# Performance work log

Hardware: AMD Instinct MI355X
Metric: run time of the kernel (lower is better)

## Reference

```python
import jax, jax.numpy as jnp
import numpy as np

B, L, R, H, TE = 4, 256, 64, 768, 100
TH = 0.5  # all four thresholds default to 0.5


def extract_first_embeddings(tok, start_probs, end_probs, threshold):
    """For each token i with start_prob>th, pair it with the nearest end index j>=i
    with end_prob>th; span embedding = mean(tok[i:j+1]). Valid spans are packed
    (in order) into a [b, l, h] table padded with zeros, with a [b, l] validity mask.
    Vectorized, jit-friendly reconstruction of the repo's span extractor."""
    b, l, h = tok.shape
    ar = jnp.arange(l)
    starts = start_probs > threshold            # [b, l]
    ends = end_probs > threshold                # [b, l]
    end_pos = jnp.where(ends, ar[None, :], l)   # l = sentinel 'no end'
    next_end = jax.lax.cummin(end_pos, axis=1, reverse=True)  # first end >= i
    valid = starts & (next_end < l)             # [b, l]
    j = jnp.minimum(next_end, l - 1)
    # inclusive span mean via prefix sums: mean = (csum[j+1] - csum[i]) / (j-i+1)
    csum0 = jnp.concatenate([jnp.zeros((b, 1, h), tok.dtype), jnp.cumsum(tok, axis=1)], axis=1)
    upper = jnp.take_along_axis(csum0, (j + 1)[:, :, None], axis=1)  # [b, l, h]
    lower = csum0[:, :-1]                                             # csum0[:, i]
    span_len = (j - ar[None, :] + 1).astype(tok.dtype)[:, :, None]
    span_emb = (upper - lower) / span_len
    # pack valid spans to the front (pad_sequence-style), pad with zeros to length l
    rank = jnp.cumsum(valid, axis=1) - 1
    rank_safe = jnp.where(valid, rank, l)       # dump invalids into extra slot l
    padded = jnp.zeros((b, l + 1, h), tok.dtype).at[
        jnp.arange(b)[:, None], rank_safe
    ].set(jnp.where(valid[:, :, None], span_emb, 0.0))[:, :l]
    num = valid.sum(axis=1)
    mask = ar[None, :] < num[:, None]
    return padded, mask


def setup_inputs() -> dict:
    key = jax.random.key(0)
    ks = jax.random.split(key, 12)
    s = 0.02
    return {
        "embs": jax.random.normal(ks[0], (B, L, H), jnp.float32),
        "h_gs": jax.random.normal(ks[1], (B, H), jnp.float32),
        "rel_embs": jax.random.normal(ks[2], (R, H), jnp.float32),
        "rel_transe_embs": jax.random.normal(ks[3], (R, TE), jnp.float32),
        "fc_w": jax.random.normal(ks[4], (8, H), jnp.float32) * s,
        "fc_b": jax.random.normal(ks[5], (8,), jnp.float32) * s,
        "Wm": jax.random.normal(ks[6], (10, H, H), jnp.float32) * s,
        "Wb": jax.random.normal(ks[7], (10, H), jnp.float32) * s,
        "V_w": jax.random.normal(ks[8], (H,), jnp.float32) * s,
        "V_b": jax.random.normal(ks[9], (1,), jnp.float32) * s,
        "rproj_w": jax.random.normal(ks[10], (TE, H), jnp.float32) * s,
        "rproj_b": jax.random.normal(ks[11], (H,), jnp.float32) * s,
    }


def _forward(embs, h_gs, rel_embs, rel_transe_embs, fc_w, fc_b, Wm, Wb, V_w, V_b, rproj_w, rproj_b):
    sig = jax.nn.sigmoid
    b_rel = rel_transe_embs @ rproj_w + rproj_b            # [r, h] r_proj

    # ---- first-stage scalar heads on tokens ----
    f_sub_s = embs @ fc_w[0] + fc_b[0]                     # [b, l]
    f_sub_e = embs @ fc_w[1] + fc_b[1]
    b_obj_s = embs @ fc_w[2] + fc_b[2]
    b_obj_e = embs @ fc_w[3] + fc_b[3]

    f_pad, f_mask = extract_first_embeddings(embs, sig(f_sub_s), sig(f_sub_e), TH)
    b_pad, b_mask = extract_first_embeddings(embs, sig(b_obj_s), sig(b_obj_e), TH)
    f_s_w = (f_pad @ Wm[0] + Wb[0]) * f_mask[:, :, None].astype(embs.dtype)  # f_W_s
    b_o_w = (b_pad @ Wm[1] + Wb[1]) * b_mask[:, :, None].astype(embs.dtype)  # b_W_s

    # ---- relation attention: tanh(W_r rel + W_g hg + W_x tok), broadcast [b,l,r,h] ----
    def rel_attn(rel, iWr, iWg, iWx):
        relp = rel @ Wm[iWr] + Wb[iWr]                     # [r, h]
        hgp = h_gs @ Wm[iWg] + Wb[iWg]                     # [b, h]
        tokp = embs @ Wm[iWx] + Wb[iWx]                    # [b, l, h]
        e = jnp.tanh(tokp[:, :, None, :] + relp[None, None, :, :] + hgp[:, None, None, :])
        v = e @ V_w + V_b                                  # [b, l, r]
        A = jax.nn.softmax(v, axis=1)                      # softmax over tokens
        C = jnp.einsum('blr,blh->brh', A, embs)            # relation context
        return C

    f_C = rel_attn(rel_embs, 2, 3, 4)
    b_C = rel_attn(b_rel, 5, 6, 7)

    # ---- pairwise table heads; Hijk = Hik[:,:,None]+C[:,None]+tok[:,:,None] is linear
    # under the scalar head, so compute logits without materializing [b,l,r,h] ----
    f_Hik = f_s_w + embs @ Wm[8] + Wb[8]                   # [b, l, h] (f_Wx2)
    b_Hik = b_o_w + embs @ Wm[9] + Wb[9]                   # (b_Wx2)

    def pair_logits(Hik, C, i):
        t = (Hik + embs) @ fc_w[i]                         # [b, l]
        return t[:, :, None] + (C @ fc_w[i])[:, None, :] + fc_b[i]  # [b, l, r]

    f_obj_s = pair_logits(f_Hik, f_C, 4)
    f_obj_e = pair_logits(f_Hik, f_C, 5)
    b_sub_s = pair_logits(b_Hik, b_C, 6)
    b_sub_e = pair_logits(b_Hik, b_C, 7)

    # order: forward(sub_s, sub_e, obj_s, obj_e), backward(obj_s, obj_e, sub_s, sub_e)
    return (f_sub_s, f_sub_e, f_obj_s, f_obj_e, b_obj_s, b_obj_e, b_sub_s, b_sub_e)


def reference(embs, h_gs, rel_embs, rel_transe_embs, fc_w, fc_b, Wm, Wb, V_w, V_b, rproj_w, rproj_b):
    return _forward(embs, h_gs, rel_embs, rel_transe_embs, fc_w, fc_b, Wm, Wb, V_w, V_b, rproj_w, rproj_b)
```

## Files before the change

### kernel.cpp

```cpp
#include <hip/hip_runtime.h>
#include <cstddef>

using u16 = unsigned short;
typedef __attribute__((ext_vector_type(8))) short bf16x8;
typedef __attribute__((ext_vector_type(4))) short bf16x4;
typedef __attribute__((ext_vector_type(4))) float f32x4;

constexpr int kB = 4, kL = 256, kR = 64, kH = 768, kTE = 100;
constexpr size_t HH = (size_t)kH * kH;

constexpr size_t OFF_FSS = 0;
constexpr size_t OFF_FSE = OFF_FSS + kB * kL;
constexpr size_t OFF_FOS = OFF_FSE + kB * kL;
constexpr size_t OFF_FOE = OFF_FOS + (size_t)kB * kL * kR;
constexpr size_t OFF_BOS = OFF_FOE + (size_t)kB * kL * kR;
constexpr size_t OFF_BOE = OFF_BOS + kB * kL;
constexpr size_t OFF_BSS = OFF_BOE + kB * kL;
constexpr size_t OFF_BSE = OFF_BSS + (size_t)kB * kL * kR;

constexpr size_t WS_WTALL   = 0;
constexpr size_t WS_EMBSB   = WS_WTALL   + 10 * HH / 2;
constexpr size_t WS_RELEMBB = WS_EMBSB   + (1024 * 768) / 2;
constexpr size_t WS_HGSB    = WS_RELEMBB + (64 * 768) / 2;
constexpr size_t WS_FPADB   = WS_HGSB    + (4 * 768) / 2;
constexpr size_t WS_BPADB   = WS_FPADB   + (1024 * 768) / 2;
constexpr size_t WS_BRELB   = WS_BPADB   + (1024 * 768) / 2;
constexpr size_t WS_TOKPB   = WS_BRELB   + (64 * 768) / 2;
constexpr size_t WS_RELPF   = WS_TOKPB   + (2 * 1024 * 768) / 2;
constexpr size_t WS_RELPB   = WS_RELPF   + 64 * 768;
constexpr size_t WS_HGPF    = WS_RELPB   + 64 * 768;
constexpr size_t WS_HGPB    = WS_HGPF    + 4 * 768;
constexpr size_t WS_DD      = WS_HGPB    + 4 * 768;
constexpr size_t WS_UA      = WS_DD      + 4 * 1024;
constexpr size_t WS_UB      = WS_UA      + 4 * 768;
constexpr size_t WS_CC      = WS_UB      + 4 * 768;
constexpr size_t WS_FMASK   = WS_CC      + 8;
constexpr size_t WS_BMASK   = WS_FMASK   + 1024;
constexpr size_t WS_C4      = WS_BMASK   + 1024;
constexpr size_t WS_C5      = WS_C4 + 256;
constexpr size_t WS_C6      = WS_C5 + 256;
constexpr size_t WS_C7      = WS_C6 + 256;

__device__ inline float fast_rcp(float x) {
#if __has_builtin(__builtin_amdgcn_rcpf)
    return __builtin_amdgcn_rcpf(x);
#else
    return 1.f / x;
#endif
}
__device__ inline float fast_exp2(float x) {
#if __has_builtin(__builtin_amdgcn_exp2f)
    return __builtin_amdgcn_exp2f(x);
#else
    return __exp2f(x);
#endif
}
__device__ inline u16 f2bf(float x) {
    union { float f; unsigned u; } v; v.f = x;
    unsigned r = v.u + 0x7FFFu + ((v.u >> 16) & 1u);
    return (u16)(r >> 16);
}
__device__ inline float bf2f(u16 x) {
    union { unsigned u; float f; } v; v.u = ((unsigned)x) << 16;
    return v.f;
}

__global__ __launch_bounds__(256) void k_prep_all(
        const float* __restrict__ embs, const float* __restrict__ rel_embs,
        const float* __restrict__ h_gs, const float* __restrict__ rel_transe,
        const float* __restrict__ fc_w, const float* __restrict__ fc_b,
        const float* __restrict__ Wm, const float* __restrict__ Wb,
        const float* __restrict__ rproj_w, const float* __restrict__ rproj_b,
        float* __restrict__ out, u16* __restrict__ embsB,
        u16* __restrict__ relembB, u16* __restrict__ hgsB, u16* __restrict__ brelB,
        u16* __restrict__ WtAll,
        float* __restrict__ uA, float* __restrict__ uB, float* __restrict__ cc,
        float* __restrict__ dd)
{
    __shared__ float sh[64 * 65];
    int bx = blockIdx.x, t = threadIdx.x;
    if (bx < 1024) {
        int tok = bx;
        const float* e = embs + (size_t)tok * kH;
        float s[8] = {0, 0, 0, 0, 0, 0, 0, 0};
        for (int h = t; h < kH; h += 256) {
            float x = e[h];
            embsB[(size_t)tok * kH + h] = f2bf(x);
#pragma unroll
            for (int j = 0; j < 8; j++) s[j] += x * fc_w[j * kH + h];
        }
#pragma unroll
        for (int off = 32; off; off >>= 1)
#pragma unroll
            for (int j = 0; j < 8; j++) s[j] += __shfl_down(s[j], off, 64);
        float(*red)[4] = (float(*)[4])sh;
        int wid = t >> 6;
        if ((t & 63) == 0) {
#pragma unroll
            for (int j = 0; j < 8; j++) red[j][wid] = s[j];
        }
        __syncthreads();
        if (t == 0) {
            float r[8];
#pragma unroll
            for (int j = 0; j < 8; j++) r[j] = red[j][0] + red[j][1] + red[j][2] + red[j][3];
            out[OFF_FSS + tok] = r[0] + fc_b[0];
            out[OFF_FSE + tok] = r[1] + fc_b[1];
            out[OFF_BOS + tok] = r[2] + fc_b[2];
            out[OFF_BOE + tok] = r[3] + fc_b[3];
            dd[0 * 1024 + tok] = r[4];
            dd[1 * 1024 + tok] = r[5];
            dd[2 * 1024 + tok] = r[6];
            dd[3 * 1024 + tok] = r[7];
        }
    } else if (bx < 1888) {
        int px = bx - 1024;
        int mi = 2 + px / 144, tile = px % 144;
        int kt = (tile / 12) * 64, nt = (tile % 12) * 64;
        const float* src = Wm + (size_t)mi * HH;
        u16* dst = WtAll + (size_t)mi * HH;
        float(*tl)[65] = (float(*)[65])sh;
        int r = t >> 2, cq = (t & 3) * 16;
        int row = kt + r;
#pragma unroll
        for (int q = 0; q < 4; q++) {
            float4 v = *(const float4*)(src + (size_t)row * kH + nt + cq + q * 4);
            tl[r][cq + q * 4 + 0] = v.x;
            tl[r][cq + q * 4 + 1] = v.y;
            tl[r][cq + q * 4 + 2] = v.z;
            tl[r][cq + q * 4 + 3] = v.w;
        }
        __syncthreads();
        u16* drow = dst + (size_t)(nt + r) * kH + kt + cq;
#pragma unroll
        for (int j = 0; j < 16; j++) drow[j] = f2bf(tl[cq + j][r]);
    } else if (bx < 2656) {
        int gx = bx - 1888;
        int p = gx / 192;
        int wid = t >> 6, lane = t & 63;
        int row = (gx % 192) * 4 + wid;
        const int wmI[4] = {0, 1, 8, 9};
        const float* W  = Wm + (size_t)wmI[p] * HH + (size_t)row * kH;
        const float* wa = fc_w + (size_t)((p & 1) ? 6 : 4) * kH;
        const float* wb = wa + kH;
        float sa = 0.f, sb = 0.f;
        for (int c = lane; c < kH; c += 64) {
            float wv = W[c];
            sa += wv * wa[c];
            sb += wv * wb[c];
        }
#pragma unroll
        for (int off = 32; off; off >>= 1) {
            sa += __shfl_xor(sa, off, 64);
            sb += __shfl_xor(sb, off, 64);
        }
        if (lane == 0) {
            if (p < 2) {
                uA[(2 * p) * kH + row]     = sa;
                uA[(2 * p + 1) * kH + row] = sb;
            } else {
                int q = p - 2;
                uB[(2 * q) * kH + row]     = sa + wa[row];
                uB[(2 * q + 1) * kH + row] = sb + wb[row];
            }
        }
    } else if (bx < 2720) {
        int r = bx - 2656;
        for (int h = t; h < kH; h += 256) relembB[r * kH + h] = f2bf(rel_embs[r * kH + h]);
    } else if (bx < 2724) {
        int r = bx - 2720;
        for (int h = t; h < kH; h += 256) hgsB[r * kH + h] = f2bf(h_gs[r * kH + h]);
    } else if (bx < 2788) {
        int r = bx - 2724;
        if (t < kTE) sh[t] = rel_transe[r * kTE + t];
        __syncthreads();
        float a0 = rproj_b[t], a1 = rproj_b[t + 256], a2 = rproj_b[t + 512];
        for (int k = 0; k < kTE; k++) {
            float rv = sh[k];
            const float* wr = rproj_w + (size_t)k * kH;
            a0 = fmaf(rv, wr[t], a0);
            a1 = fmaf(rv, wr[t + 256], a1);
            a2 = fmaf(rv, wr[t + 512], a2);
        }
        brelB[r * kH + t]       = f2bf(a0);
        brelB[r * kH + t + 256] = f2bf(a1);
        brelB[r * kH + t + 512] = f2bf(a2);
    } else {
        int j = bx - 2788;
        const int wbI[8] = {0, 0, 1, 1, 8, 8, 9, 9};
        const int fcI[8] = {4, 5, 6, 7, 4, 5, 6, 7};
        const float* wb = Wb + (size_t)wbI[j] * kH;
        const float* w  = fc_w + (size_t)fcI[j] * kH;
        float s = 0.f;
        for (int h = t; h < kH; h += 256) s += wb[h] * w[h];
#pragma unroll
        for (int off = 32; off; off >>= 1) s += __shfl_down(s, off, 64);
        int wid = t >> 6;
        if ((t & 63) == 0) sh[wid] = s;
        __syncthreads();
        if (t == 0) cc[j] = sh[0] + sh[1] + sh[2] + sh[3];
    }
}

struct GemmJob {
    const u16* A; const u16* Wt; const float* bias;
    float* C; u16* Cbf; const float* rowmask;
    int M; int K; int ldc; int coff;
};
struct GemmBatch { GemmJob j[6]; };

__device__ inline int swz(int row, int slot) {
    return row * 64 + ((slot ^ (row & 7)) << 3);
}

__global__ __launch_bounds__(256) void k_span_gemm(GemmBatch batch,
        const float* __restrict__ out, const float* __restrict__ embs,
        float* __restrict__ fmask, float* __restrict__ bmask,
        u16* __restrict__ fpadB, u16* __restrict__ bpadB)
{
    __shared__ short Als[2][64 * 64];
    __shared__ short Bls[2][64 * 64];
    int bx = blockIdx.x;
    if (bx < 2048) {
        int which = bx >> 10;
        int b = (bx >> 8) & 3;
        int i0 = bx & 255;
        int i = threadIdx.x;
        const float* slog = out + (which ? OFF_BOS : OFF_FSS) + (size_t)b * kL;
        const float* elog = out + (which ? OFF_BOE : OFF_FSE) + (size_t)b * kL;
        float sv = slog[i], ev = elog[i];
        bool st = (1.f / (1.f + __expf(-sv)) > 0.5f);
        bool en = (1.f / (1.f + __expf(-ev)) > 0.5f);

        int* sm = (int*)(&Als[0][0]);
        int* ps = sm + kL;
        sm[i] = en ? i : kL;
        __syncthreads();
        for (int step = 1; step < kL; step <<= 1) {
            int v = (i + step < kL) ? sm[i + step] : kL;
            __syncthreads();
            sm[i] = min(sm[i], v);
            __syncthreads();
        }
        int next_end = sm[i];
        ps[i] = (st && next_end < kL) ? 1 : 0;
        __syncthreads();
        for (int step = 1; step < kL; step <<= 1) {
            int v = (i >= step) ? ps[i - step] : 0;
            __syncthreads();
            ps[i] += v;
            __syncthreads();
        }
        __shared__ int meta[3];
        if (i == i0) {
            int valid0 = (st && next_end < kL) ? 1 : 0;
            meta[0] = valid0;
            meta[1] = min(next_end, kL - 1);
            meta[2] = ps[i0] - 1;
            int num = ps[kL - 1];
            (which ? bmask : fmask)[b * kL + i0] = (i0 < num) ? 1.f : 0.f;
        }
        __syncthreads();
        if (!meta[0]) return;
        int j = meta[1];
        int rk = meta[2];
        int len = j - i0 + 1;
        float inv = 1.f / (float)len;
        u16* pad = (which ? bpadB : fpadB) + ((size_t)(b * kL + rk)) * kH;
        const float* e = embs + ((size_t)(b * kL + i0)) * kH;
        for (int h = threadIdx.x; h < kH; h += 256) {
            float s = 0.f;
            for (int row = 0; row < len; row++) s += e[(size_t)row * kH + h];
            pad[h] = f2bf(s * inv);
        }
        return;
    }
    int g = bx - 2048;
    int jz, mx, ny;
    if (g < 48)       { jz = g / 12;            mx = 0;              ny = g % 12; }
    else if (g < 240) { jz = 4;                 mx = (g - 48) / 12;  ny = (g - 48) % 12; }
    else              { jz = 5;                 mx = (g - 240) / 12; ny = (g - 240) % 12; }
    GemmJob jb = batch.j[jz];

    int tid = threadIdx.x;
    int m0 = mx * 64;
    int n0 = ny * 64;
    int w = tid >> 6, lane = tid & 63;
    int wm = (w >> 1) * 32, wn = (w & 1) * 32;
    int lrow = lane & 15, lhi = lane >> 4;
    int srow = tid >> 2, sc0 = tid & 3;
    int K = jb.K;
    int T = K >> 6;

    f32x4 zero4 = {0.f, 0.f, 0.f, 0.f};
    f32x4 acc[2][2];
#pragma unroll
    for (int i = 0; i < 2; i++)
#pragma unroll
        for (int j = 0; j < 2; j++) acc[i][j] = zero4;

    bf16x8 pa[2], pb[2];

#define LOADT(k0)                                                                 \
    {                                                                             \
        _Pragma("unroll")                                                         \
        for (int q = 0; q < 2; q++) {                                             \
            bf16x8 va;                                                            \
            _Pragma("unroll") for (int z = 0; z < 8; z++) va[z] = 0;              \
            if (m0 + srow < jb.M)                                                 \
                va = *reinterpret_cast<const bf16x8*>(                            \
                    jb.A + (size_t)(m0 + srow) * K + (k0) + (sc0 + q * 4) * 8);   \
            pa[q] = va;                                                           \
            pb[q] = *reinterpret_cast<const bf16x8*>(                             \
                jb.Wt + (size_t)(n0 + srow) * K + (k0) + (sc0 + q * 4) * 8);      \
        }                                                                         \
    }
#define STORET(buf)                                                               \
    {                                                                             \
        _Pragma("unroll")                                                         \
        for (int q = 0; q < 2; q++) {                                             \
            *reinterpret_cast<bf16x8*>(&Als[buf][swz(srow, sc0 + q * 4)]) = pa[q];\
            *reinterpret_cast<bf16x8*>(&Bls[buf][swz(srow, sc0 + q * 4)]) = pb[q];\
        }                                                                         \
    }

    LOADT(0);
    STORET(0);
    __syncthreads();
    int cur = 0;
    for (int t = 0; t < T; t++) {
        if (t + 1 < T) LOADT((t + 1) << 6);
#pragma unroll
        for (int sub = 0; sub < 2; sub++) {
            bf16x8 af[2], bg[2];
#pragma unroll
            for (int i = 0; i < 2; i++) {
                af[i] = *reinterpret_cast<const bf16x8*>(
                    &Als[cur][swz(wm + i * 16 + lrow, sub * 4 + lhi)]);
                bg[i] = *reinterpret_cast<const bf16x8*>(
                    &Bls[cur][swz(wn + i * 16 + lrow, sub * 4 + lhi)]);
            }
#pragma unroll
            for (int i = 0; i < 2; i++)
#pragma unroll
                for (int j = 0; j < 2; j++)
                    acc[i][j] = __builtin_amdgcn_mfma_f32_16x16x32_bf16(af[i], bg[j], acc[i][j], 0, 0, 0);
        }
        if (t + 1 < T) STORET(cur ^ 1);
        __syncthreads();
        cur ^= 1;
    }
#undef LOADT
#undef STORET

#pragma unroll
    for (int i = 0; i < 2; i++) {
#pragma unroll
        for (int j = 0; j < 2; j++) {
            int n = n0 + wn + j * 16 + lrow;
            float bi = jb.bias[n];
#pragma unroll
            for (int q = 0; q < 4; q++) {
                int m = m0 + wm + i * 16 + lhi * 4 + q;
                if (m < jb.M) {
                    float val = acc[i][j][q] + bi;
                    if (jb.rowmask) val = (jb.rowmask[m] != 0.f) ? val : 0.f;
                    if (jb.C)   jb.C[(size_t)m * jb.ldc + jb.coff + n] = val;
                    if (jb.Cbf) jb.Cbf[(size_t)m * jb.ldc + jb.coff + n] = f2bf(val);
                }
            }
        }
    }
}

__global__ __launch_bounds__(512) void k_score(const u16* __restrict__ tokpB,
        const float* __restrict__ relpf, const float* __restrict__ relpb,
        const float* __restrict__ hgpf, const float* __restrict__ hgpb,
        const float* __restrict__ V_w, const float* __restrict__ V_b,
        const float* __restrict__ dd,
        float* __restrict__ c4, float* __restrict__ c5,
        float* __restrict__ c6, float* __restrict__ c7)
{
    constexpr float C = 2.8853900817779268f;
    int idx = blockIdx.x;
    int which = idx >> 8, b = (idx >> 6) & 3, r = idx & 63;
    int tid = threadIdx.x;
    int wid = tid >> 6, lane = tid & 63;
    int h0 = lane * 12;
    const float* relp = (which ? relpb : relpf) + (size_t)r * kH + h0;
    const float* hgp  = (which ? hgpb : hgpf) + (size_t)b * kH + h0;
    const float* vw   = V_w + h0;

    __shared__ float sc[kL];
    __shared__ float red2[2][8];

    float av2[12], w2[12], wsum = 0.f;
#pragma unroll
    for (int j = 0; j < 12; j++) {
        av2[j] = C * (relp[j] + hgp[j]);
        float wv = vw[j];
        w2[j] = -2.f * wv;
        wsum += wv;
    }
    float vb = V_b[0];
    const u16* base = tokpB + ((size_t)which * (kB * kL) + b * kL) * kH + h0;

    int l0 = wid * 32;
    bf16x4 t0 = *reinterpret_cast<const bf16x4*>(base + (size_t)l0 * kH);
    bf16x4 t1 = *reinterpret_cast<const bf16x4*>(base + (size_t)l0 * kH + 4);
    bf16x4 t2 = *reinterpret_cast<const bf16x4*>(base + (size_t)l0 * kH + 8);
    for (int l = l0; l < l0 + 32; l++) {
        bf16x4 n0, n1, n2;
        if (l + 1 < l0 + 32) {
            const u16* nrow = base + (size_t)(l + 1) * kH;
            n0 = *reinterpret_cast<const bf16x4*>(nrow);
            n1 = *reinterpret_cast<const bf16x4*>(nrow + 4);
            n2 = *reinterpret_cast<const bf16x4*>(nrow + 8);
        }
        float acc = wsum;
#pragma unroll
        for (int j = 0; j < 4; j++) {
            float e0 = fast_exp2(fmaf(bf2f((u16)t0[j]), C, av2[j]));
            acc = fmaf(w2[j], fast_rcp(e0 + 1.f), acc);
            float e1 = fast_exp2(fmaf(bf2f((u16)t1[j]), C, av2[4 + j]));
            acc = fmaf(w2[4 + j], fast_rcp(e1 + 1.f), acc);
            float e2 = fast_exp2(fmaf(bf2f((u16)t2[j]), C, av2[8 + j]));
            acc = fmaf(w2[8 + j], fast_rcp(e2 + 1.f), acc);
        }
#pragma unroll
        for (int off = 32; off; off >>= 1) acc += __shfl_xor(acc, off, 64);
        if (lane == 0) sc[l] = acc + vb;
        t0 = n0; t1 = n1; t2 = n2;
    }
    __syncthreads();

    int l = tid & 255;
    bool act = tid < 256;
    float x = act ? sc[l] : -3.4e38f;
    float m = x;
#pragma unroll
    for (int off = 32; off; off >>= 1) m = fmaxf(m, __shfl_xor(m, off, 64));
    if (lane == 0) red2[0][wid] = m;
    __syncthreads();
    m = fmaxf(fmaxf(red2[0][0], red2[0][1]), fmaxf(red2[0][2], red2[0][3]));
    float p = act ? __expf(x - m) : 0.f;
    float s = p;
#pragma unroll
    for (int off = 32; off; off >>= 1) s += __shfl_xor(s, off, 64);
    __syncthreads();
    if (lane == 0) red2[0][wid] = s;
    __syncthreads();
    s = red2[0][0] + red2[0][1] + red2[0][2] + red2[0][3];
    float a = p / s;
    const float* dA = dd + (size_t)(which ? 2 : 0) * 1024 + b * 256;
    const float* dB = dd + (size_t)(which ? 3 : 1) * 1024 + b * 256;
    float q0 = act ? a * dA[l] : 0.f;
    float q1 = act ? a * dB[l] : 0.f;
#pragma unroll
    for (int off = 32; off; off >>= 1) {
        q0 += __shfl_xor(q0, off, 64);
        q1 += __shfl_xor(q1, off, 64);
    }
    __syncthreads();
    if (lane == 0) { red2[0][wid] = q0; red2[1][wid] = q1; }
    __syncthreads();
    if (tid == 0) {
        float r0 = red2[0][0] + red2[0][1] + red2[0][2] + red2[0][3];
        float r1 = red2[1][0] + red2[1][1] + red2[1][2] + red2[1][3];
        if (which) { c6[b * kR + r] = r0; c7[b * kR + r] = r1; }
        else       { c4[b * kR + r] = r0; c5[b * kR + r] = r1; }
    }
}

__global__ __launch_bounds__(256) void k_t_final(const float* __restrict__ embs,
        const u16* __restrict__ fpadB, const u16* __restrict__ bpadB,
        const float* __restrict__ uA, const float* __restrict__ uB,
        const float* __restrict__ cc,
        const float* __restrict__ fmask, const float* __restrict__ bmask,
        const float* __restrict__ c4, const float* __restrict__ c5,
        const float* __restrict__ c6, const float* __restrict__ c7,
        const float* __restrict__ fc_b, float* __restrict__ out)
{
    int t = blockIdx.x;
    int b = t >> 8;
    size_t base = (size_t)t * kH;
    float a4 = 0, a5 = 0, a6 = 0, a7 = 0, f4 = 0, f5 = 0, b6 = 0, b7 = 0;
    for (int h = threadIdx.x; h < kH; h += 256) {
        float e = embs[base + h];
        a4 += e * uB[h];
        a5 += e * uB[kH + h];
        a6 += e * uB[2 * kH + h];
        a7 += e * uB[3 * kH + h];
        float fp = bf2f(fpadB[base + h]);
        f4 += fp * uA[h];
        f5 += fp * uA[kH + h];
        float bp = bf2f(bpadB[base + h]);
        b6 += bp * uA[2 * kH + h];
        b7 += bp * uA[3 * kH + h];
    }
#pragma unroll
    for (int off = 32; off; off >>= 1) {
        a4 += __shfl_down(a4, off, 64);
        a5 += __shfl_down(a5, off, 64);
        a6 += __shfl_down(a6, off, 64);
        a7 += __shfl_down(a7, off, 64);
        f4 += __shfl_down(f4, off, 64);
        f5 += __shfl_down(f5, off, 64);
        b6 += __shfl_down(b6, off, 64);
        b7 += __shfl_down(b7, off, 64);
    }
    __shared__ float red[8][4];
    __shared__ float fin[4];
    int wid = threadIdx.x >> 6;
    if ((threadIdx.x & 63) == 0) {
        red[0][wid] = a4; red[1][wid] = a5; red[2][wid] = a6; red[3][wid] = a7;
        red[4][wid] = f4; red[5][wid] = f5; red[6][wid] = b6; red[7][wid] = b7;
    }
    __syncthreads();
    if (threadIdx.x == 0) {
        float ra4 = red[0][0] + red[0][1] + red[0][2] + red[0][3];
        float ra5 = red[1][0] + red[1][1] + red[1][2] + red[1][3];
        float ra6 = red[2][0] + red[2][1] + red[2][2] + red[2][3];
        float ra7 = red[3][0] + red[3][1] + red[3][2] + red[3][3];
        float rf4 = red[4][0] + red[4][1] + red[4][2] + red[4][3];
        float rf5 = red[5][0] + red[5][1] + red[5][2] + red[5][3];
        float rb6 = red[6][0] + red[6][1] + red[6][2] + red[6][3];
        float rb7 = red[7][0] + red[7][1] + red[7][2] + red[7][3];
        bool mf = fmask[t] != 0.f, mb = bmask[t] != 0.f;
        fin[0] = (mf ? (rf4 + cc[0]) : 0.f) + ra4 + cc[4];
        fin[1] = (mf ? (rf5 + cc[1]) : 0.f) + ra5 + cc[5];
        fin[2] = (mb ? (rb6 + cc[2]) : 0.f) + ra6 + cc[6];
        fin[3] = (mb ? (rb7 + cc[3]) : 0.f) + ra7 + cc[7];
    }
    __syncthreads();
    int row = threadIdx.x >> 6, r = threadIdx.x & 63;
    const float* cp = (row == 0) ? c4 : (row == 1) ? c5 : (row == 2) ? c6 : c7;
    size_t off = (row == 0) ? OFF_FOS : (row == 1) ? OFF_FOE : (row == 2) ? OFF_BSS : OFF_BSE;
    out[off + (size_t)t * kR + r] = fin[row] + cp[b * kR + r] + fc_b[4 + row];
}

extern "C" void kernel_launch(void* const* d_in, const int* in_sizes, int n_in,
                              void* d_out, int out_size, void* d_ws, size_t ws_size,
                              hipStream_t stream)
{
    const float* embs       = (const float*)d_in[0];
    const float* h_gs       = (const float*)d_in[1];
    const float* rel_embs   = (const float*)d_in[2];
    const float* rel_transe = (const float*)d_in[3];
    const float* fc_w       = (const float*)d_in[4];
    const float* fc_b       = (const float*)d_in[5];
    const float* Wm         = (const float*)d_in[6];
    const float* Wb         = (const float*)d_in[7];
    const float* V_w        = (const float*)d_in[8];
    const float* V_b        = (const float*)d_in[9];
    const float* rproj_w    = (const float*)d_in[10];
    const float* rproj_b    = (const float*)d_in[11];
    float* out = (float*)d_out;
    float* ws  = (float*)d_ws;

    u16* WtAll   = (u16*)(ws + WS_WTALL);
    u16* embsB   = (u16*)(ws + WS_EMBSB);
    u16* relembB = (u16*)(ws + WS_RELEMBB);
    u16* hgsB    = (u16*)(ws + WS_HGSB);
    u16* fpadB   = (u16*)(ws + WS_FPADB);
    u16* bpadB   = (u16*)(ws + WS_BPADB);
    u16* brelB   = (u16*)(ws + WS_BRELB);
    u16* tokpB   = (u16*)(ws + WS_TOKPB);
    float* relpf = ws + WS_RELPF;
    float* relpb = ws + WS_RELPB;
    float* hgpf  = ws + WS_HGPF;
    float* hgpb  = ws + WS_HGPB;
    float* dd    = ws + WS_DD;
    float* uA    = ws + WS_UA;
    float* uB    = ws + WS_UB;
    float* cc    = ws + WS_CC;
    float* fmask = ws + WS_FMASK;
    float* bmask = ws + WS_BMASK;
    float* c4 = ws + WS_C4; float* c5 = ws + WS_C5;
    float* c6 = ws + WS_C6; float* c7 = ws + WS_C7;

    k_prep_all<<<2796, 256, 0, stream>>>(embs, rel_embs, h_gs, rel_transe,
        fc_w, fc_b, Wm, Wb, rproj_w, rproj_b,
        out, embsB, relembB, hgsB, brelB, WtAll, uA, uB, cc, dd);

    {
        GemmBatch bt;
        bt.j[0] = { relembB, WtAll + 2 * HH, Wb + 2 * kH, relpf, nullptr, nullptr, kR, kH, kH, 0 };
        bt.j[1] = { hgsB,    WtAll + 3 * HH, Wb + 3 * kH, hgpf,  nullptr, nullptr, kB, kH, kH, 0 };
        bt.j[2] = { hgsB,    WtAll + 6 * HH, Wb + 6 * kH, hgpb,  nullptr, nullptr, kB, kH, kH, 0 };
        bt.j[3] = { brelB,   WtAll + 5 * HH, Wb + 5 * kH, relpb, nullptr, nullptr, kR, kH, kH, 0 };
        bt.j[4] = { embsB,   WtAll + 4 * HH, Wb + 4 * kH, nullptr, tokpB,            nullptr, kB * kL, kH, kH, 0 };
        bt.j[5] = { embsB,   WtAll + 7 * HH, Wb + 7 * kH, nullptr, tokpB + (size_t)kB * kL * kH, nullptr, kB * kL, kH, kH, 0 };
        k_span_gemm<<<2480, 256, 0, stream>>>(bt, out, embs, fmask, bmask, fpadB, bpadB);
    }

    k_score<<<512, 512, 0, stream>>>(tokpB, relpf, relpb, hgpf, hgpb, V_w, V_b,
                                     dd, c4, c5, c6, c7);

    k_t_final<<<kB * kL, 256, 0, stream>>>(embs, fpadB, bpadB, uA, uB, cc, fmask, bmask,
                                           c4, c5, c6, c7, fc_b, out);
}
```

Measured before the change: 78.70 us.

## Replace span-table materialization with scalar prefix-sum projections and fuse final head

```diff
diff --git a/kernel.cpp b/kernel.cpp
--- a/kernel.cpp
+++ b/kernel.cpp
@@ -22,9 +22,7 @@
 constexpr size_t WS_EMBSB   = WS_WTALL   + 10 * HH / 2;
 constexpr size_t WS_RELEMBB = WS_EMBSB   + (1024 * 768) / 2;
 constexpr size_t WS_HGSB    = WS_RELEMBB + (64 * 768) / 2;
-constexpr size_t WS_FPADB   = WS_HGSB    + (4 * 768) / 2;
-constexpr size_t WS_BPADB   = WS_FPADB   + (1024 * 768) / 2;
-constexpr size_t WS_BRELB   = WS_BPADB   + (1024 * 768) / 2;
+constexpr size_t WS_BRELB   = WS_HGSB    + (4 * 768) / 2;
 constexpr size_t WS_TOKPB   = WS_BRELB   + (64 * 768) / 2;
 constexpr size_t WS_RELPF   = WS_TOKPB   + (2 * 1024 * 768) / 2;
 constexpr size_t WS_RELPB   = WS_RELPF   + 64 * 768;
@@ -34,12 +32,10 @@
 constexpr size_t WS_UA      = WS_DD      + 4 * 1024;
 constexpr size_t WS_UB      = WS_UA      + 4 * 768;
 constexpr size_t WS_CC      = WS_UB      + 4 * 768;
-constexpr size_t WS_FMASK   = WS_CC      + 8;
-constexpr size_t WS_BMASK   = WS_FMASK   + 1024;
-constexpr size_t WS_C4      = WS_BMASK   + 1024;
-constexpr size_t WS_C5      = WS_C4 + 256;
-constexpr size_t WS_C6      = WS_C5 + 256;
-constexpr size_t WS_C7      = WS_C6 + 256;
+constexpr size_t WS_T4      = WS_CC      + 8;
+constexpr size_t WS_T5      = WS_T4 + 1024;
+constexpr size_t WS_T6      = WS_T5 + 1024;
+constexpr size_t WS_T7      = WS_T6 + 1024;
 
 __device__ inline float fast_rcp(float x) {
 #if __has_builtin(__builtin_amdgcn_rcpf)
@@ -213,27 +209,30 @@
     return row * 64 + ((slot ^ (row & 7)) << 3);
 }
 
-__global__ __launch_bounds__(256) void k_span_gemm(GemmBatch batch,
+__global__ __launch_bounds__(256) void k_scan_gemm(GemmBatch batch,
         const float* __restrict__ out, const float* __restrict__ embs,
-        float* __restrict__ fmask, float* __restrict__ bmask,
-        u16* __restrict__ fpadB, u16* __restrict__ bpadB)
+        const float* __restrict__ uA, const float* __restrict__ uB,
+        const float* __restrict__ cc,
+        float* __restrict__ t4, float* __restrict__ t5,
+        float* __restrict__ t6, float* __restrict__ t7)
 {
     __shared__ short Als[2][64 * 64];
     __shared__ short Bls[2][64 * 64];
     int bx = blockIdx.x;
-    if (bx < 2048) {
-        int which = bx >> 10;
-        int b = (bx >> 8) & 3;
-        int i0 = bx & 255;
+    if (bx < 8) {
+        int which = bx >> 2, b = bx & 3;
         int i = threadIdx.x;
         const float* slog = out + (which ? OFF_BOS : OFF_FSS) + (size_t)b * kL;
         const float* elog = out + (which ? OFF_BOE : OFF_FSE) + (size_t)b * kL;
-        float sv = slog[i], ev = elog[i];
-        bool st = (1.f / (1.f + __expf(-sv)) > 0.5f);
-        bool en = (1.f / (1.f + __expf(-ev)) > 0.5f);
-
-        int* sm = (int*)(&Als[0][0]);
-        int* ps = sm + kL;
+        bool st = slog[i] > 0.f;
+        bool en = elog[i] > 0.f;
+
+        int* sm   = (int*)&Als[0][0];
+        int* ps   = sm + kL;
+        float* PA0 = (float*)(ps + kL);
+        float* PA1 = PA0 + kL;
+        float* pv0 = PA1 + kL;
+        float* pv1 = pv0 + kL;
         sm[i] = en ? i : kL;
         __syncthreads();
         for (int step = 1; step < kL; step <<= 1) {
@@ -243,7 +242,8 @@
             __syncthreads();
         }
         int next_end = sm[i];
-        ps[i] = (st && next_end < kL) ? 1 : 0;
+        int validi = (st && next_end < kL) ? 1 : 0;
+        ps[i] = validi;
         __syncthreads();
         for (int step = 1; step < kL; step <<= 1) {
             int v = (i >= step) ? ps[i - step] : 0;
@@ -251,31 +251,51 @@
             ps[i] += v;
             __syncthreads();
         }
-        __shared__ int meta[3];
-        if (i == i0) {
-            int valid0 = (st && next_end < kL) ? 1 : 0;
-            meta[0] = valid0;
-            meta[1] = min(next_end, kL - 1);
-            meta[2] = ps[i0] - 1;
-            int num = ps[kL - 1];
-            (which ? bmask : fmask)[b * kL + i0] = (i0 < num) ? 1.f : 0.f;
-        }
-        __syncthreads();
-        if (!meta[0]) return;
-        int j = meta[1];
-        int rk = meta[2];
-        int len = j - i0 + 1;
-        float inv = 1.f / (float)len;
-        u16* pad = (which ? bpadB : fpadB) + ((size_t)(b * kL + rk)) * kH;
-        const float* e = embs + ((size_t)(b * kL + i0)) * kH;
-        for (int h = threadIdx.x; h < kH; h += 256) {
-            float s = 0.f;
-            for (int row = 0; row < len; row++) s += e[(size_t)row * kH + h];
-            pad[h] = f2bf(s * inv);
-        }
+        int p0 = which ? 2 : 0, p1 = p0 + 1;
+        const float* e   = embs + (size_t)(b * kL + i) * kH;
+        const float* ua0 = uA + (size_t)p0 * kH;
+        const float* ua1 = uA + (size_t)p1 * kH;
+        const float* ub0 = uB + (size_t)p0 * kH;
+        const float* ub1 = uB + (size_t)p1 * kH;
+        float da0 = 0, da1 = 0, db0 = 0, db1 = 0;
+        for (int h = 0; h < kH; h++) {
+            float x = e[h];
+            da0 = fmaf(x, ua0[h], da0);
+            da1 = fmaf(x, ua1[h], da1);
+            db0 = fmaf(x, ub0[h], db0);
+            db1 = fmaf(x, ub1[h], db1);
+        }
+        PA0[i] = da0; PA1[i] = da1;
+        __syncthreads();
+        for (int step = 1; step < kL; step <<= 1) {
+            float v0 = (i >= step) ? PA0[i - step] : 0.f;
+            float v1 = (i >= step) ? PA1[i - step] : 0.f;
+            __syncthreads();
+            PA0[i] += v0; PA1[i] += v1;
+            __syncthreads();
+        }
+        pv0[i] = 0.f; pv1[i] = 0.f;
+        __syncthreads();
+        if (validi) {
+            int j = next_end;
+            int rk = ps[i] - 1;
+            float inv = 1.f / (float)(j - i + 1);
+            float lo0 = i ? PA0[i - 1] : 0.f;
+            float lo1 = i ? PA1[i - 1] : 0.f;
+            pv0[rk] = (PA0[j] - lo0) * inv;
+            pv1[rk] = (PA1[j] - lo1) * inv;
+        }
+        __syncthreads();
+        int num = ps[kL - 1];
+        float cp0 = cc[p0], cp1 = cc[p1];
+        float ce0 = cc[4 + p0], ce1 = cc[4 + p1];
+        float v0 = ((i < num) ? (pv0[i] + cp0) : 0.f) + db0 + ce0;
+        float v1 = ((i < num) ? (pv1[i] + cp1) : 0.f) + db1 + ce1;
+        if (which) { t6[b * kL + i] = v0; t7[b * kL + i] = v1; }
+        else       { t4[b * kL + i] = v0; t5[b * kL + i] = v1; }
         return;
     }
-    int g = bx - 2048;
+    int g = bx - 8;
     int jz, mx, ny;
     if (g < 48)       { jz = g / 12;            mx = 0;              ny = g % 12; }
     else if (g < 240) { jz = 4;                 mx = (g - 48) / 12;  ny = (g - 48) % 12; }
@@ -377,9 +397,10 @@
         const float* __restrict__ relpf, const float* __restrict__ relpb,
         const float* __restrict__ hgpf, const float* __restrict__ hgpb,
         const float* __restrict__ V_w, const float* __restrict__ V_b,
-        const float* __restrict__ dd,
-        float* __restrict__ c4, float* __restrict__ c5,
-        float* __restrict__ c6, float* __restrict__ c7)
+        const float* __restrict__ dd, const float* __restrict__ fc_b,
+        const float* __restrict__ t4, const float* __restrict__ t5,
+        const float* __restrict__ t6, const float* __restrict__ t7,
+        float* __restrict__ outp)
 {
     constexpr float C = 2.8853900817779268f;
     int idx = blockIdx.x;
@@ -464,79 +485,18 @@
     __syncthreads();
     if (lane == 0) { red2[0][wid] = q0; red2[1][wid] = q1; }
     __syncthreads();
-    if (tid == 0) {
-        float r0 = red2[0][0] + red2[0][1] + red2[0][2] + red2[0][3];
-        float r1 = red2[1][0] + red2[1][1] + red2[1][2] + red2[1][3];
-        if (which) { c6[b * kR + r] = r0; c7[b * kR + r] = r1; }
-        else       { c4[b * kR + r] = r0; c5[b * kR + r] = r1; }
-    }
-}
-
-__global__ __launch_bounds__(256) void k_t_final(const float* __restrict__ embs,
-        const u16* __restrict__ fpadB, const u16* __restrict__ bpadB,
-        const float* __restrict__ uA, const float* __restrict__ uB,
-        const float* __restrict__ cc,
-        const float* __restrict__ fmask, const float* __restrict__ bmask,
-        const float* __restrict__ c4, const float* __restrict__ c5,
-        const float* __restrict__ c6, const float* __restrict__ c7,
-        const float* __restrict__ fc_b, float* __restrict__ out)
-{
-    int t = blockIdx.x;
-    int b = t >> 8;
-    size_t base = (size_t)t * kH;
-    float a4 = 0, a5 = 0, a6 = 0, a7 = 0, f4 = 0, f5 = 0, b6 = 0, b7 = 0;
-    for (int h = threadIdx.x; h < kH; h += 256) {
-        float e = embs[base + h];
-        a4 += e * uB[h];
-        a5 += e * uB[kH + h];
-        a6 += e * uB[2 * kH + h];
-        a7 += e * uB[3 * kH + h];
-        float fp = bf2f(fpadB[base + h]);
-        f4 += fp * uA[h];
-        f5 += fp * uA[kH + h];
-        float bp = bf2f(bpadB[base + h]);
-        b6 += bp * uA[2 * kH + h];
-        b7 += bp * uA[3 * kH + h];
-    }
-#pragma unroll
-    for (int off = 32; off; off >>= 1) {
-        a4 += __shfl_down(a4, off, 64);
-        a5 += __shfl_down(a5, off, 64);
-        a6 += __shfl_down(a6, off, 64);
-        a7 += __shfl_down(a7, off, 64);
-        f4 += __shfl_down(f4, off, 64);
-        f5 += __shfl_down(f5, off, 64);
-        b6 += __shfl_down(b6, off, 64);
-        b7 += __shfl_down(b7, off, 64);
-    }
-    __shared__ float red[8][4];
-    __shared__ float fin[4];
-    int wid = threadIdx.x >> 6;
-    if ((threadIdx.x & 63) == 0) {
-        red[0][wid] = a4; red[1][wid] = a5; red[2][wid] = a6; red[3][wid] = a7;
-        red[4][wid] = f4; red[5][wid] = f5; red[6][wid] = b6; red[7][wid] = b7;
-    }
-    __syncthreads();
-    if (threadIdx.x == 0) {
-        float ra4 = red[0][0] + red[0][1] + red[0][2] + red[0][3];
-        float ra5 = red[1][0] + red[1][1] + red[1][2] + red[1][3];
-        float ra6 = red[2][0] + red[2][1] + red[2][2] + red[2][3];
-        float ra7 = red[3][0] + red[3][1] + red[3][2] + red[3][3];
-        float rf4 = red[4][0] + red[4][1] + red[4][2] + red[4][3];
-        float rf5 = red[5][0] + red[5][1] + red[5][2] + red[5][3];
-        float rb6 = red[6][0] + red[6][1] + red[6][2] + red[6][3];
-        float rb7 = red[7][0] + red[7][1] + red[7][2] + red[7][3];
-        bool mf = fmask[t] != 0.f, mb = bmask[t] != 0.f;
-        fin[0] = (mf ? (rf4 + cc[0]) : 0.f) + ra4 + cc[4];
-        fin[1] = (mf ? (rf5 + cc[1]) : 0.f) + ra5 + cc[5];
-        fin[2] = (mb ? (rb6 + cc[2]) : 0.f) + ra6 + cc[6];
-        fin[3] = (mb ? (rb7 + cc[3]) : 0.f) + ra7 + cc[7];
-    }
-    __syncthreads();
-    int row = threadIdx.x >> 6, r = threadIdx.x & 63;
-    const float* cp = (row == 0) ? c4 : (row == 1) ? c5 : (row == 2) ? c6 : c7;
-    size_t off = (row == 0) ? OFF_FOS : (row == 1) ? OFF_FOE : (row == 2) ? OFF_BSS : OFF_BSE;
-    out[off + (size_t)t * kR + r] = fin[row] + cp[b * kR + r] + fc_b[4 + row];
+    float cv0 = red2[0][0] + red2[0][1] + red2[0][2] + red2[0][3];
+    float cv1 = red2[1][0] + red2[1][1] + red2[1][2] + red2[1][3];
+    if (act) {
+        const float* tA = which ? t6 : t4;
+        const float* tB = which ? t7 : t5;
+        size_t o0 = which ? OFF_BSS : OFF_FOS;
+        size_t o1 = which ? OFF_BSE : OFF_FOE;
+        float fb0 = fc_b[which ? 6 : 4], fb1 = fc_b[which ? 7 : 5];
+        size_t row = (size_t)(b * kL + l);
+        outp[o0 + row * kR + r] = tA[b * kL + l] + cv0 + fb0;
+        outp[o1 + row * kR + r] = tB[b * kL + l] + cv1 + fb1;
+    }
 }
 
 extern "C" void kernel_launch(void* const* d_in, const int* in_sizes, int n_in,
@@ -562,8 +522,6 @@
     u16* embsB   = (u16*)(ws + WS_EMBSB);
     u16* relembB = (u16*)(ws + WS_RELEMBB);
     u16* hgsB    = (u16*)(ws + WS_HGSB);
-    u16* fpadB   = (u16*)(ws + WS_FPADB);
-    u16* bpadB   = (u16*)(ws + WS_BPADB);
     u16* brelB   = (u16*)(ws + WS_BRELB);
     u16* tokpB   = (u16*)(ws + WS_TOKPB);
     float* relpf = ws + WS_RELPF;
@@ -574,10 +532,8 @@
     float* uA    = ws + WS_UA;
     float* uB    = ws + WS_UB;
     float* cc    = ws + WS_CC;
-    float* fmask = ws + WS_FMASK;
-    float* bmask = ws + WS_BMASK;
-    float* c4 = ws + WS_C4; float* c5 = ws + WS_C5;
-    float* c6 = ws + WS_C6; float* c7 = ws + WS_C7;
+    float* t4 = ws + WS_T4; float* t5 = ws + WS_T5;
+    float* t6 = ws + WS_T6; float* t7 = ws + WS_T7;
 
     k_prep_all<<<2796, 256, 0, stream>>>(embs, rel_embs, h_gs, rel_transe,
         fc_w, fc_b, Wm, Wb, rproj_w, rproj_b,
@@ -591,12 +547,9 @@
         bt.j[3] = { brelB,   WtAll + 5 * HH, Wb + 5 * kH, relpb, nullptr, nullptr, kR, kH, kH, 0 };
         bt.j[4] = { embsB,   WtAll + 4 * HH, Wb + 4 * kH, nullptr, tokpB,            nullptr, kB * kL, kH, kH, 0 };
         bt.j[5] = { embsB,   WtAll + 7 * HH, Wb + 7 * kH, nullptr, tokpB + (size_t)kB * kL * kH, nullptr, kB * kL, kH, kH, 0 };
-        k_span_gemm<<<2480, 256, 0, stream>>>(bt, out, embs, fmask, bmask, fpadB, bpadB);
+        k_scan_gemm<<<440, 256, 0, stream>>>(bt, out, embs, uA, uB, cc, t4, t5, t6, t7);
     }
 
     k_score<<<512, 512, 0, stream>>>(tokpB, relpf, relpb, hgpf, hgpb, V_w, V_b,
-                                     dd, c4, c5, c6, c7);
-
-    k_t_final<<<kB * kL, 256, 0, stream>>>(embs, fpadB, bpadB, uA, uB, cc, fmask, bmask,
-                                           c4, c5, c6, c7, fc_b, out);
-}
+                                     dd, fc_b, t4, t5, t6, t7, out);
+}
```

After: 92.41 us. 1.17x slower.
